# Kernel tuning notes

Measured on AMD Instinct MI355X. Metric: run time of the kernel, lower is better.

Reference implementation:

```python
import jax, jax.numpy as jnp
import numpy as np

B, N, D = 4, 1024, 512
H, Dv, Dq = 8, 64, 64
NUM_BUCKETS = 64
LN_EPS = 1e-5


def setup_inputs() -> dict:
    key = jax.random.key(0)
    ks = jax.random.split(key, 10)
    x = jax.random.normal(ks[0], (B, N, D), dtype=jnp.float32)
    ts = jnp.sort(jax.random.randint(ks[1], (B, N), 0, 1_000_000), axis=1).astype(jnp.int64)
    cm = jnp.triu(jnp.ones((N, N), dtype=bool), k=1)  # causal: mask j > i
    pm = jnp.zeros((B, N), dtype=bool)                # no padding
    uvqk = 0.02 * jax.random.normal(ks[2], (D, 2 * H * Dv + 2 * H * Dq), dtype=jnp.float32)
    lim = float(np.sqrt(6.0 / (H * Dv + D)))
    o_w = jax.random.uniform(ks[3], (H * Dv, D), minval=-lim, maxval=lim, dtype=jnp.float32)
    o_b = jnp.zeros((D,), dtype=jnp.float32)
    ln_x_w = jnp.ones((D,), jnp.float32); ln_x_b = jnp.zeros((D,), jnp.float32)
    ln_a_w = jnp.ones((H * Dv,), jnp.float32); ln_a_b = jnp.zeros((H * Dv,), jnp.float32)
    ts_w = 0.02 * jax.random.normal(ks[4], (NUM_BUCKETS + 1,), dtype=jnp.float32)
    pos_w = 0.02 * jax.random.normal(ks[5], (2 * N - 1,), dtype=jnp.float32)
    return {"x": x, "ts": ts, "cm": cm, "pm": pm, "uvqk": uvqk, "o_w": o_w, "o_b": o_b,
            "ln_x_w": ln_x_w, "ln_x_b": ln_x_b, "ln_a_w": ln_a_w, "ln_a_b": ln_a_b,
            "ts_w": ts_w, "pos_w": pos_w}


def _layernorm(x, w, b):
    m = jnp.mean(x, axis=-1, keepdims=True)
    v = jnp.mean(jnp.square(x - m), axis=-1, keepdims=True)
    return (x - m) / jnp.sqrt(v + LN_EPS) * w + b


def _rel_bias(ts, ts_w, pos_w):
    # positional part: pb[i, j] = pos_w[j - i + N - 1], shape [N, N]
    idx = jnp.arange(N)
    pb = pos_w[idx[None, :] - idx[:, None] + N - 1]
    # bucketed time part
    ext = jnp.concatenate([ts, ts[:, N - 1:N]], axis=1)           # [B, N+1]
    diff = ext[:, 1:, None] - ext[:, None, :-1]                   # [B, N, N]
    logd = jnp.log(jnp.maximum(jnp.abs(diff), 1).astype(jnp.float32))
    bk = jnp.clip((logd / 0.301).astype(jnp.int32), 0, NUM_BUCKETS)
    return pb[None] + ts_w[bk]                                    # [B, N, N]


def reference(x, ts, cm, pm, uvqk, o_w, o_b, ln_x_w, ln_x_b, ln_a_w, ln_a_b, ts_w, pos_w):
    nx = _layernorm(x, ln_x_w, ln_x_b)                            # [B, N, D]
    out = jax.nn.silu(jnp.einsum('bnd,de->bne', nx, uvqk))        # [B, N, 2HDv+2HDq]
    u, v, q, k = jnp.split(out, [H * Dv, 2 * H * Dv, 2 * H * Dv + H * Dq], axis=-1)
    q = q.reshape(B, N, H, Dq)
    k = k.reshape(B, N, H, Dq)
    v = v.reshape(B, N, H, Dv)
    qk = jnp.einsum('bihd,bjhd->bhij', q, k) + _rel_bias(ts, ts_w, pos_w)[:, None]
    qk = jax.nn.silu(qk) / N
    qk = jnp.where(cm[None, None], 0.0, qk)          # causal mask
    qk = jnp.where(pm[:, None, None, :], 0.0, qk)    # padding mask on keys
    ao = jnp.einsum('bhij,bjhd->bihd', qk, v).reshape(B, N, H * Dv)
    ao = _layernorm(ao, ln_a_w, ln_a_b)
    u = u.reshape(B, N, H * Dv)
    y = (u * ao) @ o_w + o_b + x
    return jnp.where(pm[:, :, None], 0.0, y)
```

## Files before the change

kernel.cpp:

```cpp
#include <hip/hip_runtime.h>
#include <hip/hip_bf16.h>


typedef __attribute__((ext_vector_type(8))) short short8;
typedef __attribute__((ext_vector_type(4))) short bf4;
typedef __attribute__((ext_vector_type(4))) float floatx4;

#define MFMA_BF16 __builtin_amdgcn_mfma_f32_16x16x32_bf16

static __device__ __forceinline__ short f2bf(float f) {
  unsigned u = __builtin_bit_cast(unsigned, f);
  u = (u + 0x7fffu + ((u >> 16) & 1u)) >> 16;
  return (short)u;
}
static __device__ __forceinline__ unsigned pk_bf16(float a, float b) {
  __hip_bfloat162 h = __float22bfloat162_rn(float2{a, b});
  unsigned u;
  __builtin_memcpy(&u, &h, 4);
  return u;
}
static __device__ __forceinline__ short lo16(unsigned u) { return (short)(u & 0xffffu); }
static __device__ __forceinline__ short hi16(unsigned u) { return (short)(u >> 16); }
static __device__ __forceinline__ float bf2f(short s) {
  unsigned u = ((unsigned)(unsigned short)s) << 16;
  return __builtin_bit_cast(float, u);
}
static __device__ __forceinline__ float silu_f(float x) {
  return x / (1.f + __expf(-x));
}
static __device__ __forceinline__ void gl_lds16(const void* g, void* l) {
  __builtin_amdgcn_global_load_lds(
      (const __attribute__((address_space(1))) unsigned int*)g,
      (__attribute__((address_space(3))) unsigned int*)l, 16, 0, 0);
}

__global__ __launch_bounds__(256) void prep_kernel(
    const float* __restrict__ x, const int* __restrict__ ts,
    const float* __restrict__ uvqk, const float* __restrict__ o_w,
    const float* __restrict__ ln_x_w, const float* __restrict__ ln_x_b,
    const float* __restrict__ ts_w, const float* __restrict__ pos_w,
    short* __restrict__ nx, short* __restrict__ uvqk_t,
    short* __restrict__ o_wt, short* __restrict__ bias) {
  __shared__ float tile[32][33];
  const int id = blockIdx.x;
  const int t = threadIdx.x;
  if (id < 4096) {
    const int b = id >> 10, i = id & 1023;
    int ie = i + 1; if (ie > 1023) ie = 1023;
    const int tse = ts[(b << 10) + ie];
    const int j0 = t * 4;
    int4 tj = *(const int4*)&ts[(b << 10) + j0];
    const int* tjp = (const int*)&tj;
    float ov[4];
#pragma unroll
    for (int e = 0; e < 4; ++e) {
      int dt = tse - tjp[e];
      float ad = fabsf((float)dt);
      if (ad < 1.f) ad = 1.f;
      int bkt = (int)(__logf(ad) * (1.f / 0.301f));
      if (bkt > 64) bkt = 64;
      ov[e] = pos_w[j0 + e - i + 1023] + ts_w[bkt];
    }
    uint2 o2 = {pk_bf16(ov[0], ov[1]), pk_bf16(ov[2], ov[3])};
    *(uint2*)&bias[((size_t)id << 10) + j0] = o2;
  } else if (id < 5120) {
    const int lane = t & 63;
    const int row = ((id - 4096) << 2) + (t >> 6);
    const int c0 = lane * 8;
    const float* xr = x + (size_t)row * 512;
    float v[8];
    *(float4*)&v[0] = *(const float4*)(xr + c0);
    *(float4*)&v[4] = *(const float4*)(xr + c0 + 4);
    float s = 0.f, sq = 0.f;
#pragma unroll
    for (int e = 0; e < 8; ++e) { s += v[e]; sq += v[e] * v[e]; }
#pragma unroll
    for (int off = 32; off > 0; off >>= 1) {
      s += __shfl_xor(s, off);
      sq += __shfl_xor(sq, off);
    }
    float m = s * (1.f / 512.f);
    float var = sq * (1.f / 512.f) - m * m;
    float rinv = rsqrtf(var + 1e-5f);
    float wv[8], bv[8];
    *(float4*)&wv[0] = *(const float4*)(ln_x_w + c0);
    *(float4*)&wv[4] = *(const float4*)(ln_x_w + c0 + 4);
    *(float4*)&bv[0] = *(const float4*)(ln_x_b + c0);
    *(float4*)&bv[4] = *(const float4*)(ln_x_b + c0 + 4);
    float o[8];
#pragma unroll
    for (int e = 0; e < 8; ++e) o[e] = (v[e] - m) * rinv * wv[e] + bv[e];
    uint4 o4 = {pk_bf16(o[0], o[1]), pk_bf16(o[2], o[3]),
                pk_bf16(o[4], o[5]), pk_bf16(o[6], o[7])};
    *(uint4*)(nx + (size_t)row * 512 + c0) = o4;
  } else {
    const float* src; short* dst; int R, C, bc, br;
    if (id < 6144) {
      int idm = id - 5120;
      src = uvqk; dst = uvqk_t; R = 512; C = 2048;
      bc = (idm & 63) * 32; br = (idm >> 6) * 32;
    } else {
      int idm = id - 6144;
      src = o_w; dst = o_wt; R = 512; C = 512;
      bc = (idm & 15) * 32; br = (idm >> 4) * 32;
    }
    const int c = t & 31, r0 = t >> 5;
#pragma unroll
    for (int p = 0; p < 4; ++p) {
      int r = r0 + p * 8;
      tile[r][c] = src[(size_t)(br + r) * C + bc + c];
    }
    __syncthreads();
#pragma unroll
    for (int p = 0; p < 4; ++p) {
      int r = r0 + p * 8;
      dst[(size_t)(bc + r) * R + br + c] = f2bf(tile[c][r]);
    }
  }
}

__global__ __launch_bounds__(256) void gemm1_kernel(
    const short* __restrict__ A, const short* __restrict__ Bt,
    short* __restrict__ u_buf, short* __restrict__ vt_buf,
    short* __restrict__ q_buf, short* __restrict__ k_buf) {
  __shared__ __align__(16) short As[2][128 * 32];
  __shared__ __align__(16) short Bs[2][128 * 32];
  const int t = threadIdx.x;
  const int lane = t & 63, w = t >> 6;
  const int quad = lane >> 4, l15 = lane & 15;
  const int m0 = blockIdx.x * 128, n0 = blockIdx.y * 128;
  const int wm = (w & 1) * 64, wn = (w >> 1) * 64;
  const int lr = lane >> 2, lc = (lane & 3) * 8;
  floatx4 acc[4][4];
#pragma unroll
  for (int i = 0; i < 4; ++i)
#pragma unroll
    for (int j = 0; j < 4; ++j) acc[i][j] = (floatx4){0.f, 0.f, 0.f, 0.f};

  for (int k0 = 0; k0 < 512; k0 += 64) {
    __syncthreads();
#pragma unroll
    for (int c = 0; c < 2; ++c)
#pragma unroll
      for (int p = 0; p < 2; ++p) {
        int ra = w * 32 + p * 16;
        gl_lds16(&A[(size_t)(m0 + ra + lr) * 512 + k0 + c * 32 + lc], &As[c][ra * 32]);
        gl_lds16(&Bt[(size_t)(n0 + ra + lr) * 512 + k0 + c * 32 + lc], &Bs[c][ra * 32]);
      }
    __syncthreads();
#pragma unroll
    for (int c = 0; c < 2; ++c) {
      short8 af[4], bfr[4];
#pragma unroll
      for (int mi = 0; mi < 4; ++mi) af[mi] = *(const short8*)&As[c][(wm + mi * 16 + l15) * 32 + quad * 8];
#pragma unroll
      for (int ni = 0; ni < 4; ++ni) bfr[ni] = *(const short8*)&Bs[c][(wn + ni * 16 + l15) * 32 + quad * 8];
#pragma unroll
      for (int mi = 0; mi < 4; ++mi)
#pragma unroll
        for (int ni = 0; ni < 4; ++ni)
          acc[mi][ni] = MFMA_BF16(af[mi], bfr[ni], acc[mi][ni], 0, 0, 0);
    }
  }
  const int seg = n0 >> 9, cbase = n0 & 511;
  if (seg == 0) {
#pragma unroll
    for (int mi = 0; mi < 4; ++mi)
#pragma unroll
      for (int ni = 0; ni < 4; ++ni) {
        int row0 = m0 + wm + mi * 16 + quad * 4;
        int c = cbase + wn + ni * 16 + l15;
        float v0 = silu_f(acc[mi][ni][0]), v1 = silu_f(acc[mi][ni][1]);
        float v2 = silu_f(acc[mi][ni][2]), v3 = silu_f(acc[mi][ni][3]);
        unsigned pa = pk_bf16(v0, v1), pb = pk_bf16(v2, v3);
        u_buf[(size_t)row0 * 512 + c] = lo16(pa);
        u_buf[(size_t)(row0 + 1) * 512 + c] = hi16(pa);
        u_buf[(size_t)(row0 + 2) * 512 + c] = lo16(pb);
        u_buf[(size_t)(row0 + 3) * 512 + c] = hi16(pb);
      }
  } else if (seg == 1) {
#pragma unroll
    for (int mi = 0; mi < 4; ++mi)
#pragma unroll
      for (int ni = 0; ni < 4; ++ni) {
        int c = cbase + wn + ni * 16 + l15;
        int h = c >> 6, d = c & 63;
        int row0 = m0 + wm + mi * 16 + quad * 4;
        int b_ = row0 >> 10, nb = row0 & 1023;
        float v0 = silu_f(acc[mi][ni][0]) * (1.f / 1024.f);
        float v1 = silu_f(acc[mi][ni][1]) * (1.f / 1024.f);
        float v2 = silu_f(acc[mi][ni][2]) * (1.f / 1024.f);
        float v3 = silu_f(acc[mi][ni][3]) * (1.f / 1024.f);
        uint2 sv = {pk_bf16(v0, v1), pk_bf16(v2, v3)};
        *(uint2*)&vt_buf[(((size_t)(b_ * 8 + h) * 64 + d) << 10) + nb] = sv;
      }
  } else {
    short* dst = (seg == 2) ? q_buf : k_buf;
#pragma unroll
    for (int mi = 0; mi < 4; ++mi)
#pragma unroll
      for (int ni = 0; ni < 4; ++ni) {
        int row0 = m0 + wm + mi * 16 + quad * 4;
        int c = cbase + wn + ni * 16 + l15;
        int b_ = row0 >> 10, nb = row0 & 1023;
        size_t base = ((((size_t)(b_ * 8 + (c >> 6))) << 10) + nb) * 64 + (c & 63);
        float v0 = silu_f(acc[mi][ni][0]), v1 = silu_f(acc[mi][ni][1]);
        float v2 = silu_f(acc[mi][ni][2]), v3 = silu_f(acc[mi][ni][3]);
        unsigned pa = pk_bf16(v0, v1), pb = pk_bf16(v2, v3);
        dst[base] = lo16(pa);
        dst[base + 64] = hi16(pa);
        dst[base + 128] = lo16(pb);
        dst[base + 192] = hi16(pb);
      }
  }
}

__global__ __launch_bounds__(256, 4) void attn_kernel(
    const short* __restrict__ q_buf, const short* __restrict__ k_buf,
    const short* __restrict__ vt_buf, const short* __restrict__ bias_buf,
    short* __restrict__ ao_part) {
  __shared__ __align__(16) short q_s[64][72];
  __shared__ __align__(16) short k_s[64][72];
  __shared__ __align__(16) short vt_s[64][72];
  __shared__ __align__(16) short p_s[64][72];

  const int t = threadIdx.x;
  const int lane = t & 63, w = t >> 6;
  const int quad = lane >> 4, l15 = lane & 15;
  const int bh = blockIdx.x, pair = blockIdx.y, jh = blockIdx.z;
  const int b = bh >> 3, h = bh & 7;
  const short* qh = q_buf + (size_t)bh * 65536;
  const short* kh = k_buf + (size_t)bh * 65536;
  const short* vth = vt_buf + (size_t)bh * 65536;
  const int sr = t >> 2, sc = (t & 3) * 16;

#pragma unroll
  for (int half = 0; half < 2; ++half) {
    const int it = half ? (15 - pair) : pair;
    const int i0 = it * 64;
    {
      float4 qr0 = *(const float4*)&qh[(size_t)(i0 + sr) * 64 + sc];
      float4 qr1 = *(const float4*)&qh[(size_t)(i0 + sr) * 64 + sc + 8];
      *(float4*)&q_s[sr][sc] = qr0;
      *(float4*)&q_s[sr][sc + 8] = qr1;
    }
    float4 kr0, kr1, vr0, vr1;
    if (jh <= it) {
      int j0 = jh * 64;
      kr0 = *(const float4*)&kh[(size_t)(j0 + sr) * 64 + sc];
      kr1 = *(const float4*)&kh[(size_t)(j0 + sr) * 64 + sc + 8];
      vr0 = *(const float4*)&vth[(size_t)sr * 1024 + j0 + sc];
      vr1 = *(const float4*)&vth[(size_t)sr * 1024 + j0 + sc + 8];
    }
    floatx4 ao0 = {0.f, 0.f, 0.f, 0.f}, ao1 = ao0, ao2 = ao0, ao3 = ao0;
    for (int jt = jh; jt <= it; jt += 4) {
      const int j0 = jt * 64;
      short br[4][4];
      {
        const short* bb = &bias_buf[((size_t)(b * 1024 + i0 + w * 16 + quad * 4) << 10) + j0 + l15];
#pragma unroll
        for (int ni = 0; ni < 4; ++ni)
#pragma unroll
          for (int r2 = 0; r2 < 4; ++r2)
            br[ni][r2] = bb[((size_t)r2 << 10) + ni * 16];
      }
      __syncthreads();
      *(float4*)&k_s[sr][sc] = kr0;
      *(float4*)&k_s[sr][sc + 8] = kr1;
      *(float4*)&vt_s[sr][sc] = vr0;
      *(float4*)&vt_s[sr][sc + 8] = vr1;
      {
        int jn = (jt + 4 <= it) ? jt + 4 : jt;
        int jn0 = jn * 64;
        kr0 = *(const float4*)&kh[(size_t)(jn0 + sr) * 64 + sc];
        kr1 = *(const float4*)&kh[(size_t)(jn0 + sr) * 64 + sc + 8];
        vr0 = *(const float4*)&vth[(size_t)sr * 1024 + jn0 + sc];
        vr1 = *(const float4*)&vth[(size_t)sr * 1024 + jn0 + sc + 8];
      }
      __syncthreads();
      floatx4 s0, s1, s2, s3;
#pragma unroll
      for (int r2 = 0; r2 < 4; ++r2) {
        s0[r2] = bf2f(br[0][r2]);
        s1[r2] = bf2f(br[1][r2]);
        s2[r2] = bf2f(br[2][r2]);
        s3[r2] = bf2f(br[3][r2]);
      }
#pragma unroll
      for (int kk = 0; kk < 64; kk += 32) {
        short8 aq = *(const short8*)&q_s[w * 16 + l15][kk + quad * 8];
        s0 = MFMA_BF16(aq, *(const short8*)&k_s[0 + l15][kk + quad * 8], s0, 0, 0, 0);
        s1 = MFMA_BF16(aq, *(const short8*)&k_s[16 + l15][kk + quad * 8], s1, 0, 0, 0);
        s2 = MFMA_BF16(aq, *(const short8*)&k_s[32 + l15][kk + quad * 8], s2, 0, 0, 0);
        s3 = MFMA_BF16(aq, *(const short8*)&k_s[48 + l15][kk + quad * 8], s3, 0, 0, 0);
      }
      const bool diag = (jt == it);
      floatx4 sv[4] = {s0, s1, s2, s3};
#pragma unroll
      for (int ni = 0; ni < 4; ++ni) {
        int j_loc = ni * 16 + l15;
        float pv[4];
#pragma unroll
        for (int r2 = 0; r2 < 4; ++r2) {
          int i_loc = w * 16 + quad * 4 + r2;
          float p = silu_f(sv[ni][r2]);
          pv[r2] = (diag && j_loc > i_loc) ? 0.f : p;
        }
        unsigned pa = pk_bf16(pv[0], pv[1]), pb = pk_bf16(pv[2], pv[3]);
        int ib = w * 16 + quad * 4;
        p_s[ib][j_loc] = lo16(pa);
        p_s[ib + 1][j_loc] = hi16(pa);
        p_s[ib + 2][j_loc] = lo16(pb);
        p_s[ib + 3][j_loc] = hi16(pb);
      }
#pragma unroll
      for (int kk = 0; kk < 64; kk += 32) {
        short8 ap = *(const short8*)&p_s[w * 16 + l15][kk + quad * 8];
        ao0 = MFMA_BF16(ap, *(const short8*)&vt_s[0 + l15][kk + quad * 8], ao0, 0, 0, 0);
        ao1 = MFMA_BF16(ap, *(const short8*)&vt_s[16 + l15][kk + quad * 8], ao1, 0, 0, 0);
        ao2 = MFMA_BF16(ap, *(const short8*)&vt_s[32 + l15][kk + quad * 8], ao2, 0, 0, 0);
        ao3 = MFMA_BF16(ap, *(const short8*)&vt_s[48 + l15][kk + quad * 8], ao3, 0, 0, 0);
      }
    }
    floatx4 aov[4] = {ao0, ao1, ao2, ao3};
    short* aod = ao_part + (size_t)jh * 2097152;
#pragma unroll
    for (int ni = 0; ni < 4; ++ni) {
      int gi0 = i0 + w * 16 + quad * 4;
      int d = ni * 16 + l15;
      unsigned pa = pk_bf16(aov[ni][0], aov[ni][1]);
      unsigned pb = pk_bf16(aov[ni][2], aov[ni][3]);
      size_t base = ((size_t)(b * 1024 + gi0)) * 512 + h * 64 + d;
      aod[base] = lo16(pa);
      aod[base + 512] = hi16(pa);
      aod[base + 1024] = lo16(pb);
      aod[base + 1536] = hi16(pb);
    }
  }
}

__global__ __launch_bounds__(256) void ln_mul_kernel(
    const short* __restrict__ ao_part, const short* __restrict__ u,
    const float* __restrict__ w_, const float* __restrict__ b_,
    short* __restrict__ g) {
  const int lane = threadIdx.x & 63;
  const int row = (blockIdx.x << 2) + (threadIdx.x >> 6);
  const int c0 = lane * 8;
  short8 a0 = *(const short8*)(ao_part + (size_t)row * 512 + c0);
  short8 a1 = *(const short8*)(ao_part + 2097152 + (size_t)row * 512 + c0);
  short8 a2 = *(const short8*)(ao_part + 4194304 + (size_t)row * 512 + c0);
  short8 a3 = *(const short8*)(ao_part + 6291456 + (size_t)row * 512 + c0);
  float v[8];
#pragma unroll
  for (int e = 0; e < 8; ++e)
    v[e] = (bf2f(a0[e]) + bf2f(a1[e])) + (bf2f(a2[e]) + bf2f(a3[e]));
  float s = 0.f, sq = 0.f;
#pragma unroll
  for (int e = 0; e < 8; ++e) { s += v[e]; sq += v[e] * v[e]; }
#pragma unroll
  for (int off = 32; off > 0; off >>= 1) {
    s += __shfl_xor(s, off);
    sq += __shfl_xor(sq, off);
  }
  float m = s * (1.f / 512.f);
  float var = sq * (1.f / 512.f) - m * m;
  float rinv = rsqrtf(var + 1e-5f);
  float wv[8], bv[8];
  *(float4*)&wv[0] = *(const float4*)(w_ + c0);
  *(float4*)&wv[4] = *(const float4*)(w_ + c0 + 4);
  *(float4*)&bv[0] = *(const float4*)(b_ + c0);
  *(float4*)&bv[4] = *(const float4*)(b_ + c0 + 4);
  short8 uv = *(const short8*)(u + (size_t)row * 512 + c0);
  float o[8];
#pragma unroll
  for (int e = 0; e < 8; ++e)
    o[e] = bf2f(uv[e]) * ((v[e] - m) * rinv * wv[e] + bv[e]);
  uint4 o4 = {pk_bf16(o[0], o[1]), pk_bf16(o[2], o[3]),
              pk_bf16(o[4], o[5]), pk_bf16(o[6], o[7])};
  *(uint4*)(g + (size_t)row * 512 + c0) = o4;
}

__global__ __launch_bounds__(256) void gemm2_kernel(
    const short* __restrict__ G, const short* __restrict__ Wt,
    const float* __restrict__ o_b, const float* __restrict__ x,
    float* __restrict__ out) {
  __shared__ __align__(16) short As[2][64 * 32];
  __shared__ __align__(16) short Bs[2][64 * 32];
  const int t = threadIdx.x;
  const int lane = t & 63, w = t >> 6;
  const int quad = lane >> 4, l15 = lane & 15;
  const int m0 = blockIdx.x * 64, n0 = blockIdx.y * 64;
  const int lr = lane >> 2, lc = (lane & 3) * 8;
  floatx4 acc[4];
#pragma unroll
  for (int j = 0; j < 4; ++j) acc[j] = (floatx4){0.f, 0.f, 0.f, 0.f};

  for (int k0 = 0; k0 < 512; k0 += 64) {
    __syncthreads();
#pragma unroll
    for (int c = 0; c < 2; ++c) {
      int ra = w * 16;
      gl_lds16(&G[(size_t)(m0 + ra + lr) * 512 + k0 + c * 32 + lc], &As[c][ra * 32]);
      gl_lds16(&Wt[(size_t)(n0 + ra + lr) * 512 + k0 + c * 32 + lc], &Bs[c][ra * 32]);
    }
    __syncthreads();
#pragma unroll
    for (int c = 0; c < 2; ++c) {
      short8 af = *(const short8*)&As[c][(w * 16 + l15) * 32 + quad * 8];
#pragma unroll
      for (int ni = 0; ni < 4; ++ni) {
        short8 bfr = *(const short8*)&Bs[c][(ni * 16 + l15) * 32 + quad * 8];
        acc[ni] = MFMA_BF16(af, bfr, acc[ni], 0, 0, 0);
      }
    }
  }
#pragma unroll
  for (int ni = 0; ni < 4; ++ni)
#pragma unroll
    for (int r = 0; r < 4; ++r) {
      int row = m0 + w * 16 + quad * 4 + r;
      int c = n0 + ni * 16 + l15;
      out[(size_t)row * 512 + c] = acc[ni][r] + o_b[c] + x[(size_t)row * 512 + c];
    }
}

extern "C" void kernel_launch(void* const* d_in, const int* in_sizes, int n_in,
                              void* d_out, int out_size, void* d_ws, size_t ws_size,
                              hipStream_t stream) {
  const float* x = (const float*)d_in[0];
  const int* ts = (const int*)d_in[1];
  const float* uvqk = (const float*)d_in[4];
  const float* o_w = (const float*)d_in[5];
  const float* o_b = (const float*)d_in[6];
  const float* ln_x_w = (const float*)d_in[7];
  const float* ln_x_b = (const float*)d_in[8];
  const float* ln_a_w = (const float*)d_in[9];
  const float* ln_a_b = (const float*)d_in[10];
  const float* ts_w = (const float*)d_in[11];
  const float* pos_w = (const float*)d_in[12];
  float* out = (float*)d_out;

  char* ws = (char*)d_ws;
  short* nx = (short*)(ws + 0);
  short* uvqk_t = (short*)(ws + 4194304);
  short* o_wt = (short*)(ws + 6291456);
  short* u_buf = (short*)(ws + 6815744);
  short* q_buf = (short*)(ws + 11010048);
  short* k_buf = (short*)(ws + 15204352);
  short* vt_buf = (short*)(ws + 19398656);
  short* bias_buf = (short*)(ws + 23592960);
  short* ao_part = (short*)(ws + 31981568);
  short* g_buf = nx;

  hipLaunchKernelGGL(prep_kernel, dim3(6400), dim3(256), 0, stream,
                     x, ts, uvqk, o_w, ln_x_w, ln_x_b, ts_w, pos_w,
                     nx, uvqk_t, o_wt, bias_buf);
  hipLaunchKernelGGL(gemm1_kernel, dim3(32, 16), dim3(256), 0, stream, nx, uvqk_t, u_buf, vt_buf, q_buf, k_buf);
  hipLaunchKernelGGL(attn_kernel, dim3(32, 8, 4), dim3(256), 0, stream, q_buf, k_buf, vt_buf, bias_buf, ao_part);
  hipLaunchKernelGGL(ln_mul_kernel, dim3(1024), dim3(256), 0, stream, ao_part, u_buf, ln_a_w, ln_a_b, g_buf);
  hipLaunchKernelGGL(gemm2_kernel, dim3(64, 8), dim3(256), 0, stream, g_buf, o_wt, o_b, x, out);
}
```

Measured before the change: 141.3 us.

## Rewrite attention with 32x32 MFMA, register-resident Q and P via permlane swap

The attention kernel now uses 32x32x16 bf16 MFMA. Each wave owns 32 query rows held in registers, so the Q and P shared-memory tiles and their round trips are gone. P is repacked into MFMA operand layout with permlane32 swaps instead of being written to LDS. Query tiles grow to 128 rows (grid y halves), causally dead 32-column subtiles are skipped, and s_setprio raises priority around the compute. The cost is more registers per thread (launch bound lowered to 3 waves) and fewer blocks in the grid.

```diff
diff --git a/kernel.cpp b/kernel.cpp
--- a/kernel.cpp
+++ b/kernel.cpp
@@ -5,8 +5,10 @@
 typedef __attribute__((ext_vector_type(8))) short short8;
 typedef __attribute__((ext_vector_type(4))) short bf4;
 typedef __attribute__((ext_vector_type(4))) float floatx4;
+typedef __attribute__((ext_vector_type(16))) float floatx16;
 
 #define MFMA_BF16 __builtin_amdgcn_mfma_f32_16x16x32_bf16
+#define MFMA32 __builtin_amdgcn_mfma_f32_32x32x16_bf16
 
 static __device__ __forceinline__ short f2bf(float f) {
   unsigned u = __builtin_bit_cast(unsigned, f);
@@ -25,8 +27,36 @@
   unsigned u = ((unsigned)(unsigned short)s) << 16;
   return __builtin_bit_cast(float, u);
 }
+static __device__ __forceinline__ float bflo(unsigned u) {
+  return __builtin_bit_cast(float, u << 16);
+}
+static __device__ __forceinline__ float bfhi(unsigned u) {
+  return __builtin_bit_cast(float, u & 0xffff0000u);
+}
 static __device__ __forceinline__ float silu_f(float x) {
   return x / (1.f + __expf(-x));
+}
+static __device__ __forceinline__ void permswap(unsigned& a, unsigned& b) {
+#if __has_builtin(__builtin_amdgcn_permlane32_swap)
+  typedef __attribute__((ext_vector_type(2))) unsigned uint2v;
+  uint2v r = __builtin_amdgcn_permlane32_swap(a, b, false, false);
+  a = r[0];
+  b = r[1];
+#else
+  asm volatile("v_permlane32_swap_b32 %0, %1" : "+v"(a), "+v"(b));
+#endif
+}
+static __device__ __forceinline__ short8 mk8(unsigned a, unsigned b, unsigned c,
+                                             unsigned d) {
+  union {
+    unsigned u[4];
+    short8 s;
+  } r;
+  r.u[0] = a;
+  r.u[1] = b;
+  r.u[2] = c;
+  r.u[3] = d;
+  return r.s;
 }
 static __device__ __forceinline__ void gl_lds16(const void* g, void* l) {
   __builtin_amdgcn_global_load_lds(
@@ -215,20 +245,18 @@
   }
 }
 
-__global__ __launch_bounds__(256, 4) void attn_kernel(
+__global__ __launch_bounds__(256, 3) void attn_kernel(
     const short* __restrict__ q_buf, const short* __restrict__ k_buf,
     const short* __restrict__ vt_buf, const short* __restrict__ bias_buf,
     short* __restrict__ ao_part) {
-  __shared__ __align__(16) short q_s[64][72];
   __shared__ __align__(16) short k_s[64][72];
   __shared__ __align__(16) short vt_s[64][72];
-  __shared__ __align__(16) short p_s[64][72];
 
   const int t = threadIdx.x;
   const int lane = t & 63, w = t >> 6;
-  const int quad = lane >> 4, l15 = lane & 15;
-  const int bh = blockIdx.x, pair = blockIdx.y, jh = blockIdx.z;
-  const int b = bh >> 3, h = bh & 7;
+  const int l31 = lane & 31, hh = lane >> 5, h8 = hh * 8;
+  const int bh = blockIdx.x, y4 = blockIdx.y, jh = blockIdx.z;
+  const int b = bh >> 3, hd = bh & 7;
   const short* qh = q_buf + (size_t)bh * 65536;
   const short* kh = k_buf + (size_t)bh * 65536;
   const short* vth = vt_buf + (size_t)bh * 65536;
@@ -236,33 +264,89 @@
 
 #pragma unroll
   for (int half = 0; half < 2; ++half) {
-    const int it = half ? (15 - pair) : pair;
-    const int i0 = it * 64;
+    const int it = half ? (7 - y4) : y4;
+    const int i0 = it * 128;
+    const int iw0 = i0 + w * 32;
+    const int ig = iw0 + l31;
+    const int jtmax = 2 * it + 1;
+    short8 qf[4];
+#pragma unroll
+    for (int kk = 0; kk < 4; ++kk)
+      qf[kk] = *(const short8*)&qh[(size_t)ig * 64 + kk * 16 + h8];
+    const short* brow = bias_buf + (((size_t)(b * 1024 + ig)) << 10);
+    float4 kr0, kr1, vr0, vr1;
     {
-      float4 qr0 = *(const float4*)&qh[(size_t)(i0 + sr) * 64 + sc];
-      float4 qr1 = *(const float4*)&qh[(size_t)(i0 + sr) * 64 + sc + 8];
-      *(float4*)&q_s[sr][sc] = qr0;
-      *(float4*)&q_s[sr][sc + 8] = qr1;
-    }
-    float4 kr0, kr1, vr0, vr1;
-    if (jh <= it) {
       int j0 = jh * 64;
       kr0 = *(const float4*)&kh[(size_t)(j0 + sr) * 64 + sc];
       kr1 = *(const float4*)&kh[(size_t)(j0 + sr) * 64 + sc + 8];
       vr0 = *(const float4*)&vth[(size_t)sr * 1024 + j0 + sc];
       vr1 = *(const float4*)&vth[(size_t)sr * 1024 + j0 + sc + 8];
     }
-    floatx4 ao0 = {0.f, 0.f, 0.f, 0.f}, ao1 = ao0, ao2 = ao0, ao3 = ao0;
-    for (int jt = jh; jt <= it; jt += 4) {
-      const int j0 = jt * 64;
-      short br[4][4];
-      {
-        const short* bb = &bias_buf[((size_t)(b * 1024 + i0 + w * 16 + quad * 4) << 10) + j0 + l15];
-#pragma unroll
-        for (int ni = 0; ni < 4; ++ni)
-#pragma unroll
-          for (int r2 = 0; r2 < 4; ++r2)
-            br[ni][r2] = bb[((size_t)r2 << 10) + ni * 16];
+    floatx16 ao0, ao1;
+#pragma unroll
+    for (int r = 0; r < 16; ++r) { ao0[r] = 0.f; ao1[r] = 0.f; }
+
+    auto sub_tile = [&](const uint2* bw, int jcol, int jb, bool needmask) {
+      floatx16 s;
+#pragma unroll
+      for (int g = 0; g < 4; ++g) {
+        s[4 * g + 0] = bflo(bw[g].x);
+        s[4 * g + 1] = bfhi(bw[g].x);
+        s[4 * g + 2] = bflo(bw[g].y);
+        s[4 * g + 3] = bfhi(bw[g].y);
+      }
+#pragma unroll
+      for (int kk = 0; kk < 4; ++kk) {
+        short8 ak = *(const short8*)&k_s[jcol + l31][kk * 16 + h8];
+        s = MFMA32(ak, qf[kk], s, 0, 0, 0);
+      }
+      float p[16];
+#pragma unroll
+      for (int r = 0; r < 16; ++r) {
+        float xv = s[r];
+        float pv = xv / (1.f + __expf(-xv));
+        if (needmask) {
+          int jg = jb + hh * 4 + (r & 3) + 8 * (r >> 2);
+          if (jg > ig) pv = 0.f;
+        }
+        p[r] = pv;
+      }
+      unsigned X0 = pk_bf16(p[0], p[1]), Y0 = pk_bf16(p[2], p[3]);
+      unsigned X1 = pk_bf16(p[4], p[5]), Y1 = pk_bf16(p[6], p[7]);
+      unsigned X2 = pk_bf16(p[8], p[9]), Y2 = pk_bf16(p[10], p[11]);
+      unsigned X3 = pk_bf16(p[12], p[13]), Y3 = pk_bf16(p[14], p[15]);
+      permswap(X0, X1);
+      permswap(Y0, Y1);
+      permswap(X2, X3);
+      permswap(Y2, Y3);
+      short8 pa0 = mk8(X0, Y0, X1, Y1);
+      short8 pa1 = mk8(X2, Y2, X3, Y3);
+#pragma unroll
+      for (int c = 0; c < 2; ++c) {
+        short8 pa = c ? pa1 : pa0;
+        short8 bv0 = *(const short8*)&vt_s[l31][jcol + c * 16 + h8];
+        short8 bv1 = *(const short8*)&vt_s[32 + l31][jcol + c * 16 + h8];
+        ao0 = MFMA32(pa, bv0, ao0, 0, 0, 0);
+        ao1 = MFMA32(pa, bv1, ao1, 0, 0, 0);
+      }
+    };
+
+    for (int jt = jh; jt <= jtmax; jt += 4) {
+      const int j0a = jt * 64, j0b = j0a + 32;
+      const bool live_a = (j0a <= iw0 + 31);
+      const bool live_b = (j0b <= iw0 + 31);
+      const bool mask_a = live_a && (j0a + 31 > iw0);
+      const bool mask_b = live_b && (j0b + 31 > iw0);
+      uint2 bwa[4], bwb[4];
+      if (live_a) {
+#pragma unroll
+        for (int g = 0; g < 4; ++g)
+          bwa[g] = *(const uint2*)&brow[j0a + g * 8 + hh * 4];
+      }
+      if (live_b) {
+#pragma unroll
+        for (int g = 0; g < 4; ++g)
+          bwb[g] = *(const uint2*)&brow[j0b + g * 8 + hh * 4];
       }
       __syncthreads();
       *(float4*)&k_s[sr][sc] = kr0;
@@ -270,7 +354,7 @@
       *(float4*)&vt_s[sr][sc] = vr0;
       *(float4*)&vt_s[sr][sc + 8] = vr1;
       {
-        int jn = (jt + 4 <= it) ? jt + 4 : jt;
+        int jn = (jt + 4 <= jtmax) ? jt + 4 : jt;
         int jn0 = jn * 64;
         kr0 = *(const float4*)&kh[(size_t)(jn0 + sr) * 64 + sc];
         kr1 = *(const float4*)&kh[(size_t)(jn0 + sr) * 64 + sc + 8];
@@ -278,63 +362,19 @@
         vr1 = *(const float4*)&vth[(size_t)sr * 1024 + jn0 + sc + 8];
       }
       __syncthreads();
-      floatx4 s0, s1, s2, s3;
-#pragma unroll
-      for (int r2 = 0; r2 < 4; ++r2) {
-        s0[r2] = bf2f(br[0][r2]);
-        s1[r2] = bf2f(br[1][r2]);
-        s2[r2] = bf2f(br[2][r2]);
-        s3[r2] = bf2f(br[3][r2]);
-      }
-#pragma unroll
-      for (int kk = 0; kk < 64; kk += 32) {
-        short8 aq = *(const short8*)&q_s[w * 16 + l15][kk + quad * 8];
-        s0 = MFMA_BF16(aq, *(const short8*)&k_s[0 + l15][kk + quad * 8], s0, 0, 0, 0);
-        s1 = MFMA_BF16(aq, *(const short8*)&k_s[16 + l15][kk + quad * 8], s1, 0, 0, 0);
-        s2 = MFMA_BF16(aq, *(const short8*)&k_s[32 + l15][kk + quad * 8], s2, 0, 0, 0);
-        s3 = MFMA_BF16(aq, *(const short8*)&k_s[48 + l15][kk + quad * 8], s3, 0, 0, 0);
-      }
-      const bool diag = (jt == it);
-      floatx4 sv[4] = {s0, s1, s2, s3};
-#pragma unroll
-      for (int ni = 0; ni < 4; ++ni) {
-        int j_loc = ni * 16 + l15;
-        float pv[4];
-#pragma unroll
-        for (int r2 = 0; r2 < 4; ++r2) {
-          int i_loc = w * 16 + quad * 4 + r2;
-          float p = silu_f(sv[ni][r2]);
-          pv[r2] = (diag && j_loc > i_loc) ? 0.f : p;
-        }
-        unsigned pa = pk_bf16(pv[0], pv[1]), pb = pk_bf16(pv[2], pv[3]);
-        int ib = w * 16 + quad * 4;
-        p_s[ib][j_loc] = lo16(pa);
-        p_s[ib + 1][j_loc] = hi16(pa);
-        p_s[ib + 2][j_loc] = lo16(pb);
-        p_s[ib + 3][j_loc] = hi16(pb);
-      }
-#pragma unroll
-      for (int kk = 0; kk < 64; kk += 32) {
-        short8 ap = *(const short8*)&p_s[w * 16 + l15][kk + quad * 8];
-        ao0 = MFMA_BF16(ap, *(const short8*)&vt_s[0 + l15][kk + quad * 8], ao0, 0, 0, 0);
-        ao1 = MFMA_BF16(ap, *(const short8*)&vt_s[16 + l15][kk + quad * 8], ao1, 0, 0, 0);
-        ao2 = MFMA_BF16(ap, *(const short8*)&vt_s[32 + l15][kk + quad * 8], ao2, 0, 0, 0);
-        ao3 = MFMA_BF16(ap, *(const short8*)&vt_s[48 + l15][kk + quad * 8], ao3, 0, 0, 0);
-      }
-    }
-    floatx4 aov[4] = {ao0, ao1, ao2, ao3};
+      if (!live_a) continue;
+      __builtin_amdgcn_s_setprio(1);
+      sub_tile(bwa, 0, j0a, mask_a);
+      if (live_b) sub_tile(bwb, 32, j0b, mask_b);
+      __builtin_amdgcn_s_setprio(0);
+    }
     short* aod = ao_part + (size_t)jh * 2097152;
 #pragma unroll
-    for (int ni = 0; ni < 4; ++ni) {
-      int gi0 = i0 + w * 16 + quad * 4;
-      int d = ni * 16 + l15;
-      unsigned pa = pk_bf16(aov[ni][0], aov[ni][1]);
-      unsigned pb = pk_bf16(aov[ni][2], aov[ni][3]);
-      size_t base = ((size_t)(b * 1024 + gi0)) * 512 + h * 64 + d;
-      aod[base] = lo16(pa);
-      aod[base + 512] = hi16(pa);
-      aod[base + 1024] = lo16(pb);
-      aod[base + 1536] = hi16(pb);
+    for (int r = 0; r < 16; ++r) {
+      int gi = iw0 + (r & 3) + 8 * (r >> 2) + 4 * hh;
+      size_t base = ((size_t)(b * 1024 + gi)) * 512 + hd * 64 + l31;
+      aod[base] = f2bf(ao0[r]);
+      aod[base + 32] = f2bf(ao1[r]);
     }
   }
 }
@@ -456,7 +496,7 @@
                      x, ts, uvqk, o_w, ln_x_w, ln_x_b, ts_w, pos_w,
                      nx, uvqk_t, o_wt, bias_buf);
   hipLaunchKernelGGL(gemm1_kernel, dim3(32, 16), dim3(256), 0, stream, nx, uvqk_t, u_buf, vt_buf, q_buf, k_buf);
-  hipLaunchKernelGGL(attn_kernel, dim3(32, 8, 4), dim3(256), 0, stream, q_buf, k_buf, vt_buf, bias_buf, ao_part);
+  hipLaunchKernelGGL(attn_kernel, dim3(32, 4, 4), dim3(256), 0, stream, q_buf, k_buf, vt_buf, bias_buf, ao_part);
   hipLaunchKernelGGL(ln_mul_kernel, dim3(1024), dim3(256), 0, stream, ao_part, u_buf, ln_a_w, ln_a_b, g_buf);
   hipLaunchKernelGGL(gemm2_kernel, dim3(64, 8), dim3(256), 0, stream, g_buf, o_wt, o_b, x, out);
 }
```

New measurement: 147.4 us. +4.3%, slower.
